# Kernel optimization log

Hardware: AMD Instinct MI355X
Metric: run time of the kernel (lower is better)

The kernel has to match this reference:

```python
import jax, jax.numpy as jnp
import numpy as np

M = 16          # num_particles
EPS = 0.006


def setup_inputs() -> dict:
    key = jax.random.key(0)
    k1, k2, k3, k4 = jax.random.split(key, 4)
    B, P, O = 131072, 16, 4  # batch, pred_horizon, obs_horizon
    return {
        "ys_t": jax.random.normal(k1, (B, P, O), dtype=jnp.float32),
        "ys_r_stop": jax.random.normal(k2, (B, P, O), dtype=jnp.float32),
        "w_scale": jax.random.uniform(k3, (B,), dtype=jnp.float32),
        "time_weights": jax.random.uniform(k4, (B,), dtype=jnp.float32),
    }


def _laplace(a, b, ws, D):
    # a,b: [G, M, D]; ws: [G, M] (scale indexed by j, the first particle index)
    d = jnp.linalg.norm(a[:, :, None, :] - b[:, None, :, :], axis=-1)  # [G, M, M]
    d = jnp.maximum(d, EPS)
    return jnp.exp(-ws[:, :, None] * d / D)


def reference(ys_t, ys_r_stop, w_scale, time_weights):
    B = ys_t.shape[0]
    G = B // M
    x = ys_t.reshape(G, M, -1)        # [G, M, D]
    y = ys_r_stop.reshape(G, M, -1)   # [G, M, D]
    D = x.shape[-1]                   # pred_horizon * obs_horizon (dim_normalize)
    ws = w_scale.reshape(G, M)
    tw = time_weights.reshape(G, M)[:, 0]  # [G]
    terms = _laplace(x, x, ws, D) + _laplace(y, y, ws, D) - 2.0 * _laplace(x, y, ws, D)
    group_loss = terms.sum(axis=(1, 2)) * tw / (M * M)  # [G]
    return group_loss.sum() / G
```

## Files before the change

### kernel.cpp

```cpp
#include <hip/hip_runtime.h>


#define EPS_D 0.006f

#define ROT(v, O) __int_as_float(__builtin_amdgcn_update_dpp(              \
        0, __float_as_int(v), 0x120 + (O), 0xF, 0xF, false))

__device__ __forceinline__ float red4(float p) {
    p += __shfl_xor(p, 16, 64);
    p += __shfl_xor(p, 32, 64);
    return p;
}

#define UPD_FULL(O) {                                                      \
    float tx = ROT(xv, O) - xv;        \
    float tz = ROT(yv, O) - xv;                                \
    float ty = tz + dl;                                        \
    fxx[(O)-1] = fmaf(tx, tx, fxx[(O)-1]);                                 \
    fyy[(O)-1] = fmaf(ty, ty, fyy[(O)-1]);                                 \
    fxy[(O)-1] = fmaf(tz, tz, fxy[(O)-1]); }

#define UPD_XY(O) {                                                        \
    float tz = ROT(yv, O) - xv;                                            \
    gxy[(O)-8] = fmaf(tz, tz, gxy[(O)-8]); }

#define DIM_STEP(XV, YV) {                                                 \
    const float xv = (XV), yv = (YV);                                      \
    const float dl = xv - yv;                                              \
    gxy[0] = fmaf(dl, dl, gxy[0]);               \
    UPD_FULL(1) UPD_FULL(2) UPD_FULL(3) UPD_FULL(4)                        \
    UPD_FULL(5) UPD_FULL(6) UPD_FULL(7) UPD_FULL(8)                        \
    UPD_XY(9) UPD_XY(10) UPD_XY(11) UPD_XY(12)                             \
    UPD_XY(13) UPD_XY(14) UPD_XY(15) }

__global__ __launch_bounds__(256, 4)
void imm_loss_kernel(const float* __restrict__ ys_t,
                     const float* __restrict__ ys_r,
                     const float* __restrict__ w_scale,
                     const float* __restrict__ time_w,
                     float* __restrict__ partials)
{
    const int tid  = threadIdx.x;
    const int lane = tid & 63;
    const int wave = tid >> 6;
    const int q    = lane >> 4;
    const int j    = lane & 15;
    const int g    = blockIdx.x * 4 + wave;

    const size_t base = (size_t)g * 1024 + j * 64 + q * 16;
    const float4* xp = reinterpret_cast<const float4*>(ys_t + base);
    const float4* yp = reinterpret_cast<const float4*>(ys_r + base);

    float fxx[8], fyy[8], fxy[8], gxy[8];
    #pragma unroll
    for (int i = 0; i < 8; ++i) { fxx[i] = 0.f; fyy[i] = 0.f; fxy[i] = 0.f; gxy[i] = 0.f; }

    #pragma unroll
    for (int t = 0; t < 4; ++t) {
        float4 xv4 = xp[t];
        float4 yv4 = yp[t];
        DIM_STEP(xv4.x, yv4.x)
        DIM_STEP(xv4.y, yv4.y)
        DIM_STEP(xv4.z, yv4.z)
        DIM_STEP(xv4.w, yv4.w)
    }

    const float s_j = w_scale[g * 16 + j] * (1.0f / 64.0f);
    const float tw  = time_w[g * 16];

    float acc = 2.0f * __expf(-s_j * EPS_D);

    {
        float p0 = red4(gxy[0]);
        acc -= 2.0f * __expf(-s_j * fmaxf(sqrtf(p0), EPS_D));
    }

#define EPI_FULL(O, W) {                                                   \
        float pxx = red4(fxx[(O)-1]);                                      \
        float pyy = red4(fyy[(O)-1]);                                      \
        float pxy = red4(fxy[(O)-1]);                                      \
        const float s_k = ROT(s_j, O);                                     \
        const float ddx = fmaxf(sqrtf(pxx), EPS_D);                        \
        const float ddy = fmaxf(sqrtf(pyy), EPS_D);                        \
        const float ddz = fmaxf(sqrtf(pxy), EPS_D);                        \
        acc += (W) * (__expf(-s_j * ddx) + __expf(-s_k * ddx));            \
        acc += (W) * (__expf(-s_j * ddy) + __expf(-s_k * ddy));            \
        acc -= 2.0f * __expf(-s_j * ddz); }

#define EPI_XY(O) {                                                        \
        float pxy = red4(gxy[(O)-8]);                                      \
        acc -= 2.0f * __expf(-s_j * fmaxf(sqrtf(pxy), EPS_D)); }

    EPI_FULL(1, 1.0f) EPI_FULL(2, 1.0f) EPI_FULL(3, 1.0f) EPI_FULL(4, 1.0f)
    EPI_FULL(5, 1.0f) EPI_FULL(6, 1.0f) EPI_FULL(7, 1.0f) EPI_FULL(8, 0.5f)
    EPI_XY(9) EPI_XY(10) EPI_XY(11) EPI_XY(12)
    EPI_XY(13) EPI_XY(14) EPI_XY(15)

    float val = acc * tw;
    #pragma unroll
    for (int off = 32; off; off >>= 1)
        val += __shfl_xor(val, off, 64);

    __shared__ float smem[4];
    if (lane == 0) smem[wave] = val;
    __syncthreads();
    if (tid == 0)
        partials[blockIdx.x] = smem[0] + smem[1] + smem[2] + smem[3];
}

__global__ void imm_reduce_kernel(const float* __restrict__ part, int n,
                                  float inv_scale, float* __restrict__ out)
{
    const int tid = threadIdx.x;
    float v = 0.f;
    for (int i = tid; i < n; i += 256) v += part[i];
    #pragma unroll
    for (int off = 32; off; off >>= 1) v += __shfl_xor(v, off, 64);
    __shared__ float s[4];
    if ((tid & 63) == 0) s[tid >> 6] = v;
    __syncthreads();
    if (tid == 0) out[0] = (s[0] + s[1] + s[2] + s[3]) * inv_scale;
}

extern "C" void kernel_launch(void* const* d_in, const int* in_sizes, int n_in,
                              void* d_out, int out_size, void* d_ws, size_t ws_size,
                              hipStream_t stream)
{
    const float* ys_t = (const float*)d_in[0];
    const float* ys_r = (const float*)d_in[1];
    const float* wsc  = (const float*)d_in[2];
    const float* twp  = (const float*)d_in[3];
    float* out      = (float*)d_out;
    float* partials = (float*)d_ws;

    const int B = in_sizes[2];
    const int G = B / 16;
    const int blocks = G / 4;

    imm_loss_kernel<<<blocks, 256, 0, stream>>>(ys_t, ys_r, wsc, twp, partials);

    const float inv_scale = 1.0f / (4.0f * 256.0f * (float)G);
    imm_reduce_kernel<<<1, 256, 0, stream>>>(partials, blocks, inv_scale, out);
}
```

Measured before the change: 119.5 us.

## Compute pairwise distances via Gram expansion instead of difference squares

Replaces the per-dimension difference-then-square accumulation with dot-product accumulation plus per-particle squared norms, using |a-b|^2 = |a|^2 + |b|^2 - 2a·b in the epilogue. This removes the subtractions in the hot inner loop, leaving roughly one FMA per DPP-rotated value. Norms are reduced once and rotated across lanes in the epilogue. The change also lowers the launch-bounds occupancy hint from 4 to 2, which gives the compiler more register room but risks lower occupancy and adds some cancellation error in the distances.

Result: slower. 122.2 us (+2.2%).

```diff
diff --git a/kernel.cpp b/kernel.cpp
--- a/kernel.cpp
+++ b/kernel.cpp
@@ -13,27 +13,25 @@
 }
 
 #define UPD_FULL(O) {                                                      \
-    float tx = ROT(xv, O) - xv;        \
-    float tz = ROT(yv, O) - xv;                                \
-    float ty = tz + dl;                                        \
-    fxx[(O)-1] = fmaf(tx, tx, fxx[(O)-1]);                                 \
-    fyy[(O)-1] = fmaf(ty, ty, fyy[(O)-1]);                                 \
-    fxy[(O)-1] = fmaf(tz, tz, fxy[(O)-1]); }
+    axx[(O)-1] = fmaf(ROT(xv,(O)), xv, axx[(O)-1]);                        \
+    float yr = ROT(yv,(O));                                                \
+    ayy[(O)-1] = fmaf(yr, yv, ayy[(O)-1]);                                 \
+    axy[(O)]   = fmaf(yr, xv, axy[(O)]); }
 
-#define UPD_XY(O) {                                                        \
-    float tz = ROT(yv, O) - xv;                                            \
-    gxy[(O)-8] = fmaf(tz, tz, gxy[(O)-8]); }
+#define UPD_XY(O)                                                          \
+    axy[(O)] = fmaf(ROT(yv,(O)), xv, axy[(O)]);
 
 #define DIM_STEP(XV, YV) {                                                 \
     const float xv = (XV), yv = (YV);                                      \
-    const float dl = xv - yv;                                              \
-    gxy[0] = fmaf(dl, dl, gxy[0]);               \
+    sxx    = fmaf(xv, xv, sxx);                                            \
+    syy    = fmaf(yv, yv, syy);                                            \
+    axy[0] = fmaf(xv, yv, axy[0]);                                         \
     UPD_FULL(1) UPD_FULL(2) UPD_FULL(3) UPD_FULL(4)                        \
     UPD_FULL(5) UPD_FULL(6) UPD_FULL(7) UPD_FULL(8)                        \
     UPD_XY(9) UPD_XY(10) UPD_XY(11) UPD_XY(12)                             \
     UPD_XY(13) UPD_XY(14) UPD_XY(15) }
 
-__global__ __launch_bounds__(256, 4)
+__global__ __launch_bounds__(256, 2)
 void imm_loss_kernel(const float* __restrict__ ys_t,
                      const float* __restrict__ ys_r,
                      const float* __restrict__ w_scale,
@@ -51,9 +49,13 @@
     const float4* xp = reinterpret_cast<const float4*>(ys_t + base);
     const float4* yp = reinterpret_cast<const float4*>(ys_r + base);
 
-    float fxx[8], fyy[8], fxy[8], gxy[8];
+    float sxx = 0.f, syy = 0.f;
+    float axx[8], ayy[8];
+    float axy[16];
     #pragma unroll
-    for (int i = 0; i < 8; ++i) { fxx[i] = 0.f; fyy[i] = 0.f; fxy[i] = 0.f; gxy[i] = 0.f; }
+    for (int i = 0; i < 8; ++i) { axx[i] = 0.f; ayy[i] = 0.f; }
+    #pragma unroll
+    for (int i = 0; i < 16; ++i) axy[i] = 0.f;
 
     #pragma unroll
     for (int t = 0; t < 4; ++t) {
@@ -68,28 +70,36 @@
     const float s_j = w_scale[g * 16 + j] * (1.0f / 64.0f);
     const float tw  = time_w[g * 16];
 
+    const float n2x = red4(sxx);
+    const float n2y = red4(syy);
+
     float acc = 2.0f * __expf(-s_j * EPS_D);
 
     {
-        float p0 = red4(gxy[0]);
-        acc -= 2.0f * __expf(-s_j * fmaxf(sqrtf(p0), EPS_D));
+        float d2 = fmaxf(n2x + n2y - 2.0f * red4(axy[0]), 0.f);
+        acc -= 2.0f * __expf(-s_j * fmaxf(sqrtf(d2), EPS_D));
     }
 
 #define EPI_FULL(O, W) {                                                   \
-        float pxx = red4(fxx[(O)-1]);                                      \
-        float pyy = red4(fyy[(O)-1]);                                      \
-        float pxy = red4(fxy[(O)-1]);                                      \
-        const float s_k = ROT(s_j, O);                                     \
-        const float ddx = fmaxf(sqrtf(pxx), EPS_D);                        \
-        const float ddy = fmaxf(sqrtf(pyy), EPS_D);                        \
-        const float ddz = fmaxf(sqrtf(pxy), EPS_D);                        \
+        float pxx = red4(axx[(O)-1]);                                      \
+        float pyy = red4(ayy[(O)-1]);                                      \
+        float pxy = red4(axy[(O)]);                                        \
+        const float nxk = ROT(n2x, (O));                                   \
+        const float nyk = ROT(n2y, (O));                                   \
+        const float s_k = ROT(s_j, (O));                                   \
+        float d2x = fmaxf(n2x + nxk - 2.0f * pxx, 0.f);                    \
+        float d2y = fmaxf(n2y + nyk - 2.0f * pyy, 0.f);                    \
+        float d2z = fmaxf(n2x + nyk - 2.0f * pxy, 0.f);                    \
+        const float ddx = fmaxf(sqrtf(d2x), EPS_D);                        \
+        const float ddy = fmaxf(sqrtf(d2y), EPS_D);                        \
+        const float ddz = fmaxf(sqrtf(d2z), EPS_D);                        \
         acc += (W) * (__expf(-s_j * ddx) + __expf(-s_k * ddx));            \
         acc += (W) * (__expf(-s_j * ddy) + __expf(-s_k * ddy));            \
         acc -= 2.0f * __expf(-s_j * ddz); }
 
 #define EPI_XY(O) {                                                        \
-        float pxy = red4(gxy[(O)-8]);                                      \
-        acc -= 2.0f * __expf(-s_j * fmaxf(sqrtf(pxy), EPS_D)); }
+        float d2 = fmaxf(n2x + ROT(n2y,(O)) - 2.0f * red4(axy[(O)]), 0.f); \
+        acc -= 2.0f * __expf(-s_j * fmaxf(sqrtf(d2), EPS_D)); }
 
     EPI_FULL(1, 1.0f) EPI_FULL(2, 1.0f) EPI_FULL(3, 1.0f) EPI_FULL(4, 1.0f)
     EPI_FULL(5, 1.0f) EPI_FULL(6, 1.0f) EPI_FULL(7, 1.0f) EPI_FULL(8, 0.5f)
```
